# Performance work log

Hardware: AMD Instinct MI355X
Metric: run time of the kernel (lower is better)

## Reference

```python
import jax, jax.numpy as jnp
import numpy as np

EPS = 1e-09


def _glorot(key, shape):
    fan_in, fan_out = shape[-2], shape[-1]
    std = (2.0 / (fan_in + fan_out)) ** 0.5
    return jax.random.normal(key, shape, dtype=jnp.float32) * std


def setup_inputs() -> dict:
    key = jax.random.key(0)
    kx, k1, k2, k3, k4 = jax.random.split(key, 5)
    B, S, D = 2, 1024, 256
    H, K = 8, 32  # key_dim_frac = 1/8
    return {
        "x": jax.random.normal(kx, (B, S, D), dtype=jnp.float32),
        "Wks": _glorot(k1, (H, D, K)),
        "Wqs": _glorot(k2, (H, D, K)),
        "Wvs": _glorot(k3, (H, D, D)),
        "Wo": _glorot(k4, (H, D, D)),
    }


def reference(x, Wks, Wqs, Wvs, Wo):
    # Per-head projections: [H, B, S, K] / [H, B, S, D]
    keys = jnp.einsum('bsd,hdk->hbsk', x, Wks)
    queries = jnp.einsum('bsd,hdk->hbsk', x, Wqs)
    values = jnp.einsum('bsd,hde->hbse', x, Wvs)

    # Feature map: elu + 1 (strictly positive)
    keys = jax.nn.elu(keys) + 1.0
    queries = jax.nn.elu(queries) + 1.0

    # Auxiliary pairwise attention map [H, B, S, S], causal-masked, row-normalized
    att = jnp.einsum('hbsk,hbtk->hbst', queries, keys)
    S = att.shape[-1]
    causal = jnp.tril(jnp.ones((S, S), dtype=att.dtype))
    att = att * causal
    att = att / (jnp.sum(att, axis=-1, keepdims=True) + EPS)

    # Causal linear attention via cumulative sums of outer products
    # [H, B, S, D, K] cumulative state (memory-bound, mirrors tf.cumsum)
    kv = jnp.einsum('hbsk,hbsd->hbsdk', keys, values)
    kv_cum = jnp.cumsum(kv, axis=2)
    numerator = jnp.einsum('hbsdk,hbsk->hbsd', kv_cum, queries)
    denominator = jnp.einsum('hbsk,hbsk->hbs', jnp.cumsum(keys, axis=2), queries)
    node = numerator / (denominator[..., None] + EPS)

    # Output projection, summed over heads: [B, S, D]
    out = jnp.einsum('hbsd,hde->bse', node, Wo)
    return (out, att)
```

## Files before the change

kernel.cpp:

```cpp
#include <hip/hip_runtime.h>
#include <hip/hip_bf16.h>
#include <cstdio>

#define PB 2
#define PS 1024
#define PD 256
#define PK 32
#define PH 8
#define HB (PH*PB)
#define BS (PB*PS)
#define EPS 1e-9f

typedef __attribute__((ext_vector_type(8))) short bf16x8;
typedef __attribute__((ext_vector_type(4))) float f32x4;

__device__ inline unsigned short f2bf(float f) {
    __hip_bfloat16 h = __float2bfloat16(f);
    return *reinterpret_cast<unsigned short*>(&h);
}
__device__ inline float bf2f(unsigned short u) {
    return __bfloat162float(*reinterpret_cast<__hip_bfloat16*>(&u));
}

__global__ __launch_bounds__(256) void k_prep(
    const float* __restrict__ x, const float* __restrict__ Wqs,
    const float* __restrict__ Wks, const float* __restrict__ Wvs,
    const float* __restrict__ Wo,
    unsigned short* __restrict__ xb, unsigned short* __restrict__ WqT,
    unsigned short* __restrict__ WkT, unsigned short* __restrict__ WvT,
    unsigned short* __restrict__ WoT)
{
    __shared__ float smem[8448];
    int bid = blockIdx.x, tid = threadIdx.x;
    if (bid < 512) {
        int i = bid*256 + tid;
        float4 v = ((const float4*)x)[i];
        ushort4 o = {f2bf(v.x), f2bf(v.y), f2bf(v.z), f2bf(v.w)};
        ((ushort4*)xb)[i] = o;
        return;
    }
    if (bid < 528) {
        int r2 = bid - 512;
        int h = r2 >> 1, isK = r2 & 1;
        const float* S = (isK ? Wks : Wqs) + (size_t)h*8192;
        unsigned short* D = (isK ? WkT : WqT) + (size_t)h*8192;
#pragma unroll
        for (int p = 0; p < 32; ++p) {
            int idx = p*256 + tid;
            smem[(idx>>5)*33 + (idx&31)] = S[idx];
        }
        __syncthreads();
#pragma unroll
        for (int p = 0; p < 8; ++p) {
            int o4 = p*256 + tid;
            int kk = o4 >> 6, d = (o4 & 63)*4;
            ushort4 o;
            o.x = f2bf(smem[(d+0)*33 + kk]); o.y = f2bf(smem[(d+1)*33 + kk]);
            o.z = f2bf(smem[(d+2)*33 + kk]); o.w = f2bf(smem[(d+3)*33 + kk]);
            *(ushort4*)(D + (size_t)kk*256 + d) = o;
        }
        return;
    }
    int r3 = bid - 528;
    const float* S; unsigned short* dst; int rs, hs;
    if (r3 < 128) { S = Wvs; dst = WvT; rs = 256;  hs = 65536; }
    else          { r3 -= 128; S = Wo; dst = WoT; rs = 2048; hs = 256; }
    int e0 = (r3 & 3)*64, d0 = ((r3>>2) & 3)*64, h = r3 >> 4;
    float (*T)[69] = (float(*)[69])smem;
    const float* Sh = S + (size_t)h*65536;
    int ty = tid>>4, c4 = tid&15;
#pragma unroll
    for (int p = 0; p < 4; ++p) {
        int r = p*16 + ty;
        float4 v = *(const float4*)(Sh + (size_t)(d0+r)*256 + e0 + c4*4);
        T[r][c4*4+0]=v.x; T[r][c4*4+1]=v.y; T[r][c4*4+2]=v.z; T[r][c4*4+3]=v.w;
    }
    __syncthreads();
    unsigned short* D = dst + (size_t)h*hs;
#pragma unroll
    for (int p = 0; p < 4; ++p) {
        int er = p*16 + ty;
        ushort4 o;
        o.x = f2bf(T[c4*4+0][er]); o.y = f2bf(T[c4*4+1][er]);
        o.z = f2bf(T[c4*4+2][er]); o.w = f2bf(T[c4*4+3][er]);
        *(ushort4*)(D + (size_t)(e0+er)*rs + d0 + c4*4) = o;
    }
}

__global__ __launch_bounds__(256) void k_proj(
    const unsigned short* __restrict__ xb, const unsigned short* __restrict__ WqT,
    const unsigned short* __restrict__ WkT, const unsigned short* __restrict__ WvT,
    unsigned short* __restrict__ Qb, unsigned short* __restrict__ Kb,
    unsigned short* __restrict__ Vt)
{
    int z = blockIdx.z;
    int m0 = blockIdx.y*64, n0 = blockIdx.x*64;
    int tid = threadIdx.x, w = tid>>6, l15 = tid&15, g = (tid>>4)&3;
    f32x4 zf = {0.f,0.f,0.f,0.f};
    f32x4 acc[4] = {zf,zf,zf,zf};
    const unsigned short* arow = xb + (size_t)(m0+16*w+l15)*256 + 8*g;
    const unsigned short* W;
    if (z < 8)       W = WvT + (size_t)z*65536;
    else if (z == 8) W = WqT;
    else             W = WkT;
#pragma unroll
    for (int kk = 0; kk < 8; ++kk) {
        bf16x8 af = *(const bf16x8*)(arow + kk*32);
#pragma unroll
        for (int nt = 0; nt < 4; ++nt) {
            bf16x8 bf = *(const bf16x8*)(W + (size_t)(n0+16*nt+l15)*256 + kk*32 + 8*g);
            acc[nt] = __builtin_amdgcn_mfma_f32_16x16x32_bf16(af, bf, acc[nt], 0, 0, 0);
        }
    }
    if (z < 8) {
        unsigned short* VtT = Vt + ((size_t)z*32 + blockIdx.y)*(256*64);
#pragma unroll
        for (int nt = 0; nt < 4; ++nt) {
            ushort4 o = {f2bf(acc[nt][0]), f2bf(acc[nt][1]), f2bf(acc[nt][2]), f2bf(acc[nt][3])};
            *(ushort4*)(VtT + (size_t)(n0+16*nt+l15)*64 + 16*w + 4*g) = o;
        }
    } else {
        unsigned short* dst = (z == 8) ? Qb : Kb;
        int bs_base = m0 + 16*w + 4*g;
#pragma unroll
        for (int nt = 0; nt < 4; ++nt) {
            int col = n0 + 16*nt + l15;
            int h = col>>5, kk = col&31;
#pragma unroll
            for (int j = 0; j < 4; ++j) {
                int bs = bs_base + j;
                int b = bs>>10, s = bs&1023;
                float zv = acc[nt][j];
                zv = zv > 0.f ? zv + 1.f : expf(zv);
                dst[((size_t)(h*PB+b)*PS + s)*PK + kk] = f2bf(zv);
            }
        }
    }
}

__global__ __launch_bounds__(256) void k_kv_sums(
    const unsigned short* __restrict__ Kb, const unsigned short* __restrict__ Vt,
    float* __restrict__ KVs, float* __restrict__ Ksum)
{
    int c = blockIdx.x, hb = blockIdx.y;
    int tid = threadIdx.x, w = tid>>6, l15 = tid&15, g = (tid>>4)&3;
    __shared__ unsigned short KT[32*72];
    __shared__ float partial[8][32];
#pragma unroll
    for (int i = 0; i < 8; ++i) {
        int flat = tid + i*256;
        KT[(flat&31)*72 + (flat>>5)] = Kb[((size_t)hb*PS + c*64 + (flat>>5))*PK + (flat&31)];
    }
    __syncthreads();
    {
        int kk = tid & 31, part = tid >> 5;
        float s = 0.f;
#pragma unroll
        for (int i = 0; i < 8; ++i) s += bf2f(KT[kk*72 + part*8 + i]);
        partial[part][kk] = s;
    }
    const unsigned short* Vtt = Vt + ((size_t)hb*16 + c)*(256*64);
    f32x4 zf = {0.f,0.f,0.f,0.f};
    f32x4 acc[4][2];
#pragma unroll
    for (int mt = 0; mt < 4; ++mt) { acc[mt][0] = zf; acc[mt][1] = zf; }
#pragma unroll
    for (int ks = 0; ks < 2; ++ks) {
        bf16x8 af[4];
#pragma unroll
        for (int mt = 0; mt < 4; ++mt)
            af[mt] = *(const bf16x8*)(Vtt + (size_t)(64*w + 16*mt + l15)*64 + 32*ks + 8*g);
#pragma unroll
        for (int nt = 0; nt < 2; ++nt) {
            bf16x8 bf = *(const bf16x8*)(KT + (16*nt + l15)*72 + 32*ks + 8*g);
#pragma unroll
            for (int mt = 0; mt < 4; ++mt)
                acc[mt][nt] = __builtin_amdgcn_mfma_f32_16x16x32_bf16(af[mt], bf, acc[mt][nt], 0, 0, 0);
        }
    }
    __syncthreads();
    if (tid < 32) {
        float s = 0.f;
#pragma unroll
        for (int p = 0; p < 8; ++p) s += partial[p][tid];
        Ksum[((size_t)hb*16 + c)*32 + tid] = s;
    }
    float* o = KVs + ((size_t)hb*16 + c)*8192;
#pragma unroll
    for (int mt = 0; mt < 4; ++mt)
#pragma unroll
        for (int nt = 0; nt < 2; ++nt)
#pragma unroll
            for (int j = 0; j < 4; ++j)
                o[(size_t)(64*w + 16*mt + 4*g + j)*32 + 16*nt + l15] = acc[mt][nt][j];
}

__global__ void k_kv_scan(const float* __restrict__ KVs, const float* __restrict__ Ksum,
                          unsigned short* __restrict__ KVpre, float* __restrict__ Kpre) {
    int hb = blockIdx.y;
    if (blockIdx.x == 32) {
        int kk = threadIdx.x;
        if (kk < 32) {
            float acc = 0.f;
#pragma unroll
            for (int c = 0; c < 16; ++c) {
                Kpre[((size_t)hb*16 + c)*32 + kk] = acc;
                acc += Ksum[((size_t)hb*16 + c)*32 + kk];
            }
        }
        return;
    }
    int i = blockIdx.x*256 + threadIdx.x;
    const float* src = KVs + (size_t)hb*16*8192 + i;
    unsigned short* dst = KVpre + (size_t)hb*16*8192 + i;
    float acc = 0.f;
#pragma unroll
    for (int c = 0; c < 16; ++c) { dst[c*8192] = f2bf(acc); acc += src[c*8192]; }
}

__global__ __launch_bounds__(256) void k_den2(
    const unsigned short* __restrict__ Qb, const unsigned short* __restrict__ Kb,
    const float* __restrict__ Kpre, float* __restrict__ den)
{
    int c = blockIdx.x, hb = blockIdx.y;
    int tid = threadIdx.x;
    int r = tid >> 2, quad = tid & 3;
    __shared__ float kc[64][33];
    bf16x8 k8 = *(const bf16x8*)(Kb + ((size_t)hb*PS + c*64 + r)*PK + quad*8);
#pragma unroll
    for (int i = 0; i < 8; ++i) kc[r][quad*8+i] = bf2f((unsigned short)k8[i]);
    __syncthreads();
#pragma unroll
    for (int st = 1; st < 64; st <<= 1) {
        float tmp[8];
#pragma unroll
        for (int i = 0; i < 8; ++i) tmp[i] = (r >= st) ? kc[r-st][quad*8+i] : 0.f;
        __syncthreads();
#pragma unroll
        for (int i = 0; i < 8; ++i) kc[r][quad*8+i] += tmp[i];
        __syncthreads();
    }
    bf16x8 q8 = *(const bf16x8*)(Qb + ((size_t)hb*PS + c*64 + r)*PK + quad*8);
    const float* Kp = Kpre + ((size_t)hb*16 + c)*32 + quad*8;
    float p = 0.f;
#pragma unroll
    for (int i = 0; i < 8; ++i)
        p += bf2f((unsigned short)q8[i]) * (Kp[i] + kc[r][quad*8+i]);
    p += __shfl_xor(p, 1);
    p += __shfl_xor(p, 2);
    if (quad == 0) den[hb*PS + c*64 + r] = p + EPS;
}

__global__ __launch_bounds__(256) void k_att(
    const unsigned short* __restrict__ Qb, const unsigned short* __restrict__ Kb,
    const float* __restrict__ den, float* __restrict__ att)
{
    int st = blockIdx.x, hb = blockIdx.y;
    int s0 = st*64;
    int tid = threadIdx.x, w = tid>>6, l15 = tid&15, g = (tid>>4)&3;

    alignas(16) __shared__ float PT[64][68];
    __shared__ float rden[64];

    float* attb = att + (size_t)hb*PS*PS;
    int c0 = s0 + 64;
    int nzf4 = (PS - c0) >> 2;
    if (nzf4 > 0 && tid < nzf4) {
        float4 z = {0.f,0.f,0.f,0.f};
        float* zb = attb + (size_t)s0*PS + c0 + tid*4;
#pragma unroll 4
        for (int r = 0; r < 64; ++r)
            *(float4*)(zb + (size_t)r*PS) = z;
    }
    if (tid < 64) rden[tid] = 1.0f / den[hb*PS + s0 + tid];

    if (st == 0) return;

    bf16x8 qf = *(const bf16x8*)(Qb + ((size_t)hb*PS + s0 + 16*w + l15)*PK + 8*g);
    f32x4 zf = {0.f,0.f,0.f,0.f};
    __syncthreads();
    float rd[4];
#pragma unroll
    for (int j = 0; j < 4; ++j) rd[j] = rden[16*w + 4*g + j];

    for (int tt = 0; tt < st; ++tt) {
        int t0 = tt*64;
        f32x4 p[4];
#pragma unroll
        for (int nt = 0; nt < 4; ++nt) {
            bf16x8 kf = *(const bf16x8*)(Kb + ((size_t)hb*PS + t0 + 16*nt + l15)*PK + 8*g);
            p[nt] = __builtin_amdgcn_mfma_f32_16x16x32_bf16(qf, kf, zf, 0, 0, 0);
        }
#pragma unroll
        for (int nt = 0; nt < 4; ++nt)
#pragma unroll
            for (int j = 0; j < 4; ++j)
                PT[16*w + 4*g + j][16*nt + l15] = p[nt][j] * rd[j];
        __syncthreads();
#pragma unroll
        for (int pp = 0; pp < 4; ++pp) {
            int f4 = tid + pp*256;
            int r = f4 >> 4, c4 = f4 & 15;
            float4 v = *(const float4*)&PT[r][c4*4];
            *(float4*)(attb + (size_t)(s0+r)*PS + t0 + c4*4) = v;
        }
        __syncthreads();
    }
}

__global__ __launch_bounds__(256) void k_node(
    const unsigned short* __restrict__ Qb, const unsigned short* __restrict__ Kb,
    const float* __restrict__ den, const unsigned short* __restrict__ Vt,
    const unsigned short* __restrict__ KVpre,
    float* __restrict__ att, unsigned short* __restrict__ nodeB)
{
    int c = blockIdx.x, hb = blockIdx.y;
    int s0 = c*64;
    int tid = threadIdx.x, w = tid>>6, l15 = tid&15, g = (tid>>4)&3;
    __shared__ unsigned short PL[64*72];
    __shared__ float rden[64];
    if (tid < 64) rden[tid] = 1.0f / den[hb*PS + s0 + tid];

    f32x4 zf = {0.f,0.f,0.f,0.f};
    bf16x8 qf = *(const bf16x8*)(Qb + ((size_t)hb*PS + s0 + 16*w + l15)*PK + 8*g);

    const unsigned short* KVp = KVpre + ((size_t)hb*16 + c)*8192;
    f32x4 acc[16];
#pragma unroll
    for (int nt = 0; nt < 16; ++nt) {
        bf16x8 bf = *(const bf16x8*)(KVp + (size_t)(16*nt + l15)*32 + 8*g);
        acc[nt] = __builtin_amdgcn_mfma_f32_16x16x32_bf16(qf, bf, zf, 0, 0, 0);
    }
    f32x4 p[4];
#pragma unroll
    for (int nt4 = 0; nt4 < 4; ++nt4) {
        bf16x8 kf = *(const bf16x8*)(Kb + ((size_t)hb*PS + s0 + 16*nt4 + l15)*PK + 8*g);
        p[nt4] = __builtin_amdgcn_mfma_f32_16x16x32_bf16(qf, kf, zf, 0, 0, 0);
    }
    __syncthreads();
    float* attb = att + (size_t)hb*PS*PS;
#pragma unroll
    for (int nt4 = 0; nt4 < 4; ++nt4) {
#pragma unroll
        for (int j = 0; j < 4; ++j) {
            int r = 16*w + 4*g + j;
            int tc = 16*nt4 + l15;
            float v = p[nt4][j] * rden[r];
            if (tc > r) v = 0.f;
            attb[(size_t)(s0 + r)*PS + s0 + tc] = v;
            PL[r*72 + tc] = f2bf(v);
        }
    }
#pragma unroll
    for (int nt = 0; nt < 16; ++nt)
#pragma unroll
        for (int j = 0; j < 4; ++j)
            acc[nt][j] *= rden[16*w + 4*g + j];
    __syncthreads();
    const unsigned short* Vtt = Vt + ((size_t)hb*16 + c)*(256*64);
#pragma unroll
    for (int ks = 0; ks < 2; ++ks) {
        bf16x8 af = *(const bf16x8*)(PL + (size_t)(16*w + l15)*72 + 32*ks + 8*g);
#pragma unroll
        for (int nt = 0; nt < 16; ++nt) {
            bf16x8 vf = *(const bf16x8*)(Vtt + (size_t)(16*nt + l15)*64 + 32*ks + 8*g);
            acc[nt] = __builtin_amdgcn_mfma_f32_16x16x32_bf16(af, vf, acc[nt], 0, 0, 0);
        }
    }
    int h = hb >> 1, b = hb & 1;
    unsigned short* np = nodeB + ((size_t)(b*PS + s0))*2048 + h*256;
#pragma unroll
    for (int nt = 0; nt < 16; ++nt)
#pragma unroll
        for (int j = 0; j < 4; ++j)
            np[(size_t)(16*w + 4*g + j)*2048 + 16*nt + l15] = f2bf(acc[nt][j]);
}

__global__ __launch_bounds__(256) void k_out2(
    const unsigned short* __restrict__ nodeB, const unsigned short* __restrict__ WoT,
    float* __restrict__ out)
{
    int e0 = blockIdx.x*64, m0 = blockIdx.y*16;
    int tid = threadIdx.x, w = tid>>6, l15 = tid&15, g = (tid>>4)&3;
    f32x4 zf = {0.f,0.f,0.f,0.f};
    f32x4 acc = zf;
    const unsigned short* arow = nodeB + (size_t)(m0 + l15)*2048 + 8*g;
    const unsigned short* brow = WoT + (size_t)(e0 + 16*w + l15)*2048 + 8*g;
#pragma unroll 8
    for (int kk = 0; kk < 64; ++kk) {
        bf16x8 af = *(const bf16x8*)(arow + kk*32);
        bf16x8 bf = *(const bf16x8*)(brow + kk*32);
        acc = __builtin_amdgcn_mfma_f32_16x16x32_bf16(af, bf, acc, 0, 0, 0);
    }
#pragma unroll
    for (int j = 0; j < 4; ++j)
        out[(size_t)(m0 + 4*g + j)*PD + e0 + 16*w + l15] = acc[j];
}

extern "C" void kernel_launch(void* const* d_in, const int* in_sizes, int n_in,
                              void* d_out, int out_size, void* d_ws, size_t ws_size,
                              hipStream_t stream) {
    const float* x   = (const float*)d_in[0];
    const float* Wks = (const float*)d_in[1];
    const float* Wqs = (const float*)d_in[2];
    const float* Wvs = (const float*)d_in[3];
    const float* Wo  = (const float*)d_in[4];

    float* out = (float*)d_out;
    float* att = (float*)d_out + (size_t)PB*PS*PD;

    float* ws = (float*)d_ws;
    float*          den   = ws + 0;
    unsigned short* Qb    = (unsigned short*)(ws + 16384);
    unsigned short* Kb    = (unsigned short*)(ws + 278528);
    unsigned short* Vt    = (unsigned short*)(ws + 540672);
    unsigned short* xb    = (unsigned short*)(ws + 2637824);
    unsigned short* WqT   = (unsigned short*)(ws + 2899968);
    unsigned short* WkT   = (unsigned short*)(ws + 2932736);
    unsigned short* WvT   = (unsigned short*)(ws + 2965504);
    unsigned short* WoT   = (unsigned short*)(ws + 3227648);
    unsigned short* nodeB = (unsigned short*)(ws + 3489792);
    float*          KVs   = ws + 5586944;
    unsigned short* KVpre = (unsigned short*)(ws + 7684096);
    float*          KsumG = ws + 8732672;
    float*          KpreG = ws + 8740864;
    const size_t needed = (size_t)8749056 * 4;
    if (ws_size < needed) {
        fprintf(stderr, "kernel_launch: ws_size %zu < needed %zu\n", ws_size, needed);
        return;
    }

    k_prep<<<784, 256, 0, stream>>>(x, Wqs, Wks, Wvs, Wo, xb, WqT, WkT, WvT, WoT);
    k_proj<<<dim3(4, 32, 10), 256, 0, stream>>>(xb, WqT, WkT, WvT, Qb, Kb, Vt);
    k_kv_sums<<<dim3(16, HB), 256, 0, stream>>>(Kb, Vt, KVs, KsumG);
    k_kv_scan<<<dim3(33, HB), 256, 0, stream>>>(KVs, KsumG, KVpre, KpreG);
    k_den2<<<dim3(16, HB), 256, 0, stream>>>(Qb, Kb, KpreG, den);
    k_att<<<dim3(16, HB), 256, 0, stream>>>(Qb, Kb, den, att);
    k_node<<<dim3(16, HB), 256, 0, stream>>>(Qb, Kb, den, Vt, KVpre, att, nodeB);
    k_out2<<<dim3(4, 128), 256, 0, stream>>>(nodeB, WoT, out);
}
```

Baseline: 102.9 us.

## Fuse post-projection kernels into one cooperative megakernel with grid syncs

Replaces six separate launches (kv sums, kv scan, denominator, attention map, node, output projection) with a single cooperative kernel of 256 blocks of 512 threads, using grid.sync between the phases. Denominators stay in shared memory instead of going through global memory, the K prefix is computed by each block directly from the chunk sums, and the diagonal attention tile is written once alongside the bf16 copy. The intent is to remove launch overhead and inter-kernel gaps. In exchange it adds grid-wide barrier costs and a fixed, possibly poorly balanced work split, since causal attention blocks carry uneven amounts of work.

```diff
diff --git a/kernel.cpp b/kernel.cpp
--- a/kernel.cpp
+++ b/kernel.cpp
@@ -1,6 +1,9 @@
 #include <hip/hip_runtime.h>
 #include <hip/hip_bf16.h>
+#include <hip/hip_cooperative_groups.h>
 #include <cstdio>
+
+namespace cg = cooperative_groups;
 
 #define PB 2
 #define PS 1024
@@ -138,263 +141,265 @@
     }
 }
 
-__global__ __launch_bounds__(256) void k_kv_sums(
-    const unsigned short* __restrict__ Kb, const unsigned short* __restrict__ Vt,
-    float* __restrict__ KVs, float* __restrict__ Ksum)
+__global__ __launch_bounds__(512) void k_mega(
+    const unsigned short* __restrict__ Qb, const unsigned short* __restrict__ Kb,
+    const unsigned short* __restrict__ Vt,
+    float* __restrict__ KVs, float* __restrict__ KsumG,
+    unsigned short* __restrict__ KVpre,
+    float* __restrict__ att, unsigned short* __restrict__ nodeB,
+    const unsigned short* __restrict__ WoT, float* __restrict__ out)
 {
+    cg::grid_group grid = cg::this_grid();
     int c = blockIdx.x, hb = blockIdx.y;
-    int tid = threadIdx.x, w = tid>>6, l15 = tid&15, g = (tid>>4)&3;
-    __shared__ unsigned short KT[32*72];
-    __shared__ float partial[8][32];
-#pragma unroll
-    for (int i = 0; i < 8; ++i) {
-        int flat = tid + i*256;
+    int tid = threadIdx.x;
+    int w = tid >> 6, l15 = tid & 15, g = (tid >> 4) & 3;
+    f32x4 zf = {0.f, 0.f, 0.f, 0.f};
+
+    __shared__ __align__(16) unsigned char smem[26880];
+    unsigned short* PL   = (unsigned short*)smem;
+    float* rden          = (float*)(smem + 9216);
+    unsigned short* KT   = (unsigned short*)(smem + 9472);
+    float* partial       = (float*)(smem + 9472 + 4608);
+    float (*kc)[33]      = (float(*)[33])(smem + 9472);
+    float (*PT)[68]      = (float(*)[68])(smem + 9472);
+
+    const unsigned short* Vtt = Vt + ((size_t)hb*16 + c)*(256*64);
+
+#pragma unroll
+    for (int i = 0; i < 4; ++i) {
+        int flat = tid + i*512;
         KT[(flat&31)*72 + (flat>>5)] = Kb[((size_t)hb*PS + c*64 + (flat>>5))*PK + (flat&31)];
     }
     __syncthreads();
-    {
+    if (tid < 256) {
         int kk = tid & 31, part = tid >> 5;
         float s = 0.f;
 #pragma unroll
         for (int i = 0; i < 8; ++i) s += bf2f(KT[kk*72 + part*8 + i]);
-        partial[part][kk] = s;
-    }
-    const unsigned short* Vtt = Vt + ((size_t)hb*16 + c)*(256*64);
-    f32x4 zf = {0.f,0.f,0.f,0.f};
-    f32x4 acc[4][2];
-#pragma unroll
-    for (int mt = 0; mt < 4; ++mt) { acc[mt][0] = zf; acc[mt][1] = zf; }
-#pragma unroll
-    for (int ks = 0; ks < 2; ++ks) {
-        bf16x8 af[4];
-#pragma unroll
-        for (int mt = 0; mt < 4; ++mt)
-            af[mt] = *(const bf16x8*)(Vtt + (size_t)(64*w + 16*mt + l15)*64 + 32*ks + 8*g);
-#pragma unroll
-        for (int nt = 0; nt < 2; ++nt) {
-            bf16x8 bf = *(const bf16x8*)(KT + (16*nt + l15)*72 + 32*ks + 8*g);
-#pragma unroll
-            for (int mt = 0; mt < 4; ++mt)
-                acc[mt][nt] = __builtin_amdgcn_mfma_f32_16x16x32_bf16(af[mt], bf, acc[mt][nt], 0, 0, 0);
-        }
-    }
-    __syncthreads();
-    if (tid < 32) {
-        float s = 0.f;
-#pragma unroll
-        for (int p = 0; p < 8; ++p) s += partial[p][tid];
-        Ksum[((size_t)hb*16 + c)*32 + tid] = s;
-    }
-    float* o = KVs + ((size_t)hb*16 + c)*8192;
-#pragma unroll
-    for (int mt = 0; mt < 4; ++mt)
-#pragma unroll
-        for (int nt = 0; nt < 2; ++nt)
+        partial[part*32 + kk] = s;
+    }
+    {
+        f32x4 acc1[2][2];
+        acc1[0][0]=zf; acc1[0][1]=zf; acc1[1][0]=zf; acc1[1][1]=zf;
+#pragma unroll
+        for (int ks = 0; ks < 2; ++ks) {
+            bf16x8 af[2];
+#pragma unroll
+            for (int mt = 0; mt < 2; ++mt)
+                af[mt] = *(const bf16x8*)(Vtt + (size_t)(32*w + 16*mt + l15)*64 + 32*ks + 8*g);
+#pragma unroll
+            for (int nt = 0; nt < 2; ++nt) {
+                bf16x8 bf = *(const bf16x8*)(KT + (16*nt + l15)*72 + 32*ks + 8*g);
+#pragma unroll
+                for (int mt = 0; mt < 2; ++mt)
+                    acc1[mt][nt] = __builtin_amdgcn_mfma_f32_16x16x32_bf16(af[mt], bf, acc1[mt][nt], 0, 0, 0);
+            }
+        }
+        __syncthreads();
+        if (tid < 32) {
+            float s = 0.f;
+#pragma unroll
+            for (int p = 0; p < 8; ++p) s += partial[p*32 + tid];
+            KsumG[((size_t)hb*16 + c)*32 + tid] = s;
+        }
+        float* o = KVs + ((size_t)hb*16 + c)*8192;
+#pragma unroll
+        for (int mt = 0; mt < 2; ++mt)
+#pragma unroll
+            for (int nt = 0; nt < 2; ++nt)
+#pragma unroll
+                for (int j = 0; j < 4; ++j)
+                    o[(size_t)(32*w + 16*mt + 4*g + j)*32 + 16*nt + l15] = acc1[mt][nt][j];
+    }
+    grid.sync();
+
+    {
+        int i = c*512 + tid;
+        const float* src = KVs + (size_t)hb*16*8192 + i;
+        unsigned short* dst = KVpre + (size_t)hb*16*8192 + i;
+        float acc = 0.f;
+#pragma unroll
+        for (int cc = 0; cc < 16; ++cc) { dst[cc*8192] = f2bf(acc); acc += src[cc*8192]; }
+    }
+    grid.sync();
+
+    {
+        bool act = tid < 256;
+        int r = tid >> 2, quad = tid & 3;
+        if (act) {
+            bf16x8 k8 = *(const bf16x8*)(Kb + ((size_t)hb*PS + c*64 + r)*PK + quad*8);
+#pragma unroll
+            for (int i = 0; i < 8; ++i) kc[r][quad*8+i] = bf2f((unsigned short)k8[i]);
+        }
+        __syncthreads();
+#pragma unroll
+        for (int st = 1; st < 64; st <<= 1) {
+            float tmp[8];
+            if (act) {
+#pragma unroll
+                for (int i = 0; i < 8; ++i) tmp[i] = (r >= st) ? kc[r-st][quad*8+i] : 0.f;
+            }
+            __syncthreads();
+            if (act) {
+#pragma unroll
+                for (int i = 0; i < 8; ++i) kc[r][quad*8+i] += tmp[i];
+            }
+            __syncthreads();
+        }
+        if (act) {
+            float kp[8];
+#pragma unroll
+            for (int i = 0; i < 8; ++i) kp[i] = 0.f;
+            for (int cc = 0; cc < c; ++cc) {
+                const float* Ks = KsumG + ((size_t)hb*16 + cc)*32 + quad*8;
+#pragma unroll
+                for (int i = 0; i < 8; ++i) kp[i] += Ks[i];
+            }
+            bf16x8 q8 = *(const bf16x8*)(Qb + ((size_t)hb*PS + c*64 + r)*PK + quad*8);
+            float p = 0.f;
+#pragma unroll
+            for (int i = 0; i < 8; ++i)
+                p += bf2f((unsigned short)q8[i]) * (kp[i] + kc[r][quad*8+i]);
+            p += __shfl_xor(p, 1);
+            p += __shfl_xor(p, 2);
+            if (quad == 0) rden[r] = 1.0f / (p + EPS);
+        }
+        __syncthreads();
+    }
+
+    int s0 = c*64;
+    float* attb = att + (size_t)hb*PS*PS;
+    {
+        int c0 = s0 + 64;
+        int nzf4 = (PS - c0) >> 2;
+        int col = tid & 255, half = tid >> 8;
+        if (col < nzf4) {
+            float4 z = {0.f,0.f,0.f,0.f};
+            float* zb = attb + (size_t)(s0 + 32*half)*PS + c0 + col*4;
+#pragma unroll 4
+            for (int r = 0; r < 32; ++r)
+                *(float4*)(zb + (size_t)r*PS) = z;
+        }
+        int ws = w & 3, eh = w >> 2;
+        bf16x8 qf = *(const bf16x8*)(Qb + ((size_t)hb*PS + s0 + 16*ws + l15)*PK + 8*g);
+        float rd[4];
+#pragma unroll
+        for (int j = 0; j < 4; ++j) rd[j] = rden[16*ws + 4*g + j];
+        for (int tt = 0; tt < c; ++tt) {
+            int t0 = tt*64;
+            f32x4 p[2];
+#pragma unroll
+            for (int i = 0; i < 2; ++i) {
+                int nt = eh*2 + i;
+                bf16x8 kf = *(const bf16x8*)(Kb + ((size_t)hb*PS + t0 + 16*nt + l15)*PK + 8*g);
+                p[i] = __builtin_amdgcn_mfma_f32_16x16x32_bf16(qf, kf, zf, 0, 0, 0);
+            }
+#pragma unroll
+            for (int i = 0; i < 2; ++i) {
+                int nt = eh*2 + i;
+#pragma unroll
+                for (int j = 0; j < 4; ++j)
+                    PT[16*ws + 4*g + j][16*nt + l15] = p[i][j] * rd[j];
+            }
+            __syncthreads();
+#pragma unroll
+            for (int pp = 0; pp < 2; ++pp) {
+                int f4 = tid + pp*512;
+                int r = f4 >> 4, c4 = f4 & 15;
+                float4 v = *(const float4*)&PT[r][c4*4];
+                *(float4*)(attb + (size_t)(s0+r)*PS + t0 + c4*4) = v;
+            }
+            __syncthreads();
+        }
+        {
+            f32x4 p[2];
+#pragma unroll
+            for (int i = 0; i < 2; ++i) {
+                int nt = eh*2 + i;
+                bf16x8 kf = *(const bf16x8*)(Kb + ((size_t)hb*PS + s0 + 16*nt + l15)*PK + 8*g);
+                p[i] = __builtin_amdgcn_mfma_f32_16x16x32_bf16(qf, kf, zf, 0, 0, 0);
+            }
+#pragma unroll
+            for (int i = 0; i < 2; ++i) {
+                int nt = eh*2 + i;
+                int tc = 16*nt + l15;
+#pragma unroll
+                for (int j = 0; j < 4; ++j) {
+                    int r = 16*ws + 4*g + j;
+                    float v = p[i][j] * rd[j];
+                    if (tc > r) v = 0.f;
+                    PT[r][tc] = v;
+                    PL[r*72 + tc] = f2bf(v);
+                }
+            }
+            __syncthreads();
+#pragma unroll
+            for (int pp = 0; pp < 2; ++pp) {
+                int f4 = tid + pp*512;
+                int r = f4 >> 4, c4 = f4 & 15;
+                float4 v = *(const float4*)&PT[r][c4*4];
+                *(float4*)(attb + (size_t)(s0+r)*PS + s0 + c4*4) = v;
+            }
+            __syncthreads();
+        }
+    }
+
+    {
+        int ws = w & 3, eh = w >> 2;
+        bf16x8 qf = *(const bf16x8*)(Qb + ((size_t)hb*PS + s0 + 16*ws + l15)*PK + 8*g);
+        const unsigned short* KVp = KVpre + ((size_t)hb*16 + c)*8192;
+        f32x4 acc[8];
+#pragma unroll
+        for (int nt = 0; nt < 8; ++nt) {
+            int tile = eh*8 + nt;
+            bf16x8 bf = *(const bf16x8*)(KVp + (size_t)(16*tile + l15)*32 + 8*g);
+            acc[nt] = __builtin_amdgcn_mfma_f32_16x16x32_bf16(qf, bf, zf, 0, 0, 0);
+        }
+        float rd[4];
+#pragma unroll
+        for (int j = 0; j < 4; ++j) rd[j] = rden[16*ws + 4*g + j];
+#pragma unroll
+        for (int nt = 0; nt < 8; ++nt)
+#pragma unroll
+            for (int j = 0; j < 4; ++j) acc[nt][j] *= rd[j];
+#pragma unroll
+        for (int ks = 0; ks < 2; ++ks) {
+            bf16x8 af = *(const bf16x8*)(PL + (size_t)(16*ws + l15)*72 + 32*ks + 8*g);
+#pragma unroll
+            for (int nt = 0; nt < 8; ++nt) {
+                int tile = eh*8 + nt;
+                bf16x8 vf = *(const bf16x8*)(Vtt + (size_t)(16*tile + l15)*64 + 32*ks + 8*g);
+                acc[nt] = __builtin_amdgcn_mfma_f32_16x16x32_bf16(af, vf, acc[nt], 0, 0, 0);
+            }
+        }
+        int h = hb >> 1, b = hb & 1;
+        unsigned short* np = nodeB + ((size_t)(b*PS + s0))*2048 + h*256;
+#pragma unroll
+        for (int nt = 0; nt < 8; ++nt)
 #pragma unroll
             for (int j = 0; j < 4; ++j)
-                o[(size_t)(64*w + 16*mt + 4*g + j)*32 + 16*nt + l15] = acc[mt][nt][j];
-}
-
-__global__ void k_kv_scan(const float* __restrict__ KVs, const float* __restrict__ Ksum,
-                          unsigned short* __restrict__ KVpre, float* __restrict__ Kpre) {
-    int hb = blockIdx.y;
-    if (blockIdx.x == 32) {
-        int kk = threadIdx.x;
-        if (kk < 32) {
-            float acc = 0.f;
-#pragma unroll
-            for (int c = 0; c < 16; ++c) {
-                Kpre[((size_t)hb*16 + c)*32 + kk] = acc;
-                acc += Ksum[((size_t)hb*16 + c)*32 + kk];
-            }
-        }
-        return;
-    }
-    int i = blockIdx.x*256 + threadIdx.x;
-    const float* src = KVs + (size_t)hb*16*8192 + i;
-    unsigned short* dst = KVpre + (size_t)hb*16*8192 + i;
-    float acc = 0.f;
-#pragma unroll
-    for (int c = 0; c < 16; ++c) { dst[c*8192] = f2bf(acc); acc += src[c*8192]; }
-}
-
-__global__ __launch_bounds__(256) void k_den2(
-    const unsigned short* __restrict__ Qb, const unsigned short* __restrict__ Kb,
-    const float* __restrict__ Kpre, float* __restrict__ den)
-{
-    int c = blockIdx.x, hb = blockIdx.y;
-    int tid = threadIdx.x;
-    int r = tid >> 2, quad = tid & 3;
-    __shared__ float kc[64][33];
-    bf16x8 k8 = *(const bf16x8*)(Kb + ((size_t)hb*PS + c*64 + r)*PK + quad*8);
-#pragma unroll
-    for (int i = 0; i < 8; ++i) kc[r][quad*8+i] = bf2f((unsigned short)k8[i]);
-    __syncthreads();
-#pragma unroll
-    for (int st = 1; st < 64; st <<= 1) {
-        float tmp[8];
-#pragma unroll
-        for (int i = 0; i < 8; ++i) tmp[i] = (r >= st) ? kc[r-st][quad*8+i] : 0.f;
-        __syncthreads();
-#pragma unroll
-        for (int i = 0; i < 8; ++i) kc[r][quad*8+i] += tmp[i];
-        __syncthreads();
-    }
-    bf16x8 q8 = *(const bf16x8*)(Qb + ((size_t)hb*PS + c*64 + r)*PK + quad*8);
-    const float* Kp = Kpre + ((size_t)hb*16 + c)*32 + quad*8;
-    float p = 0.f;
-#pragma unroll
-    for (int i = 0; i < 8; ++i)
-        p += bf2f((unsigned short)q8[i]) * (Kp[i] + kc[r][quad*8+i]);
-    p += __shfl_xor(p, 1);
-    p += __shfl_xor(p, 2);
-    if (quad == 0) den[hb*PS + c*64 + r] = p + EPS;
-}
-
-__global__ __launch_bounds__(256) void k_att(
-    const unsigned short* __restrict__ Qb, const unsigned short* __restrict__ Kb,
-    const float* __restrict__ den, float* __restrict__ att)
-{
-    int st = blockIdx.x, hb = blockIdx.y;
-    int s0 = st*64;
-    int tid = threadIdx.x, w = tid>>6, l15 = tid&15, g = (tid>>4)&3;
-
-    alignas(16) __shared__ float PT[64][68];
-    __shared__ float rden[64];
-
-    float* attb = att + (size_t)hb*PS*PS;
-    int c0 = s0 + 64;
-    int nzf4 = (PS - c0) >> 2;
-    if (nzf4 > 0 && tid < nzf4) {
-        float4 z = {0.f,0.f,0.f,0.f};
-        float* zb = attb + (size_t)s0*PS + c0 + tid*4;
-#pragma unroll 4
-        for (int r = 0; r < 64; ++r)
-            *(float4*)(zb + (size_t)r*PS) = z;
-    }
-    if (tid < 64) rden[tid] = 1.0f / den[hb*PS + s0 + tid];
-
-    if (st == 0) return;
-
-    bf16x8 qf = *(const bf16x8*)(Qb + ((size_t)hb*PS + s0 + 16*w + l15)*PK + 8*g);
-    f32x4 zf = {0.f,0.f,0.f,0.f};
-    __syncthreads();
-    float rd[4];
-#pragma unroll
-    for (int j = 0; j < 4; ++j) rd[j] = rden[16*w + 4*g + j];
-
-    for (int tt = 0; tt < st; ++tt) {
-        int t0 = tt*64;
-        f32x4 p[4];
-#pragma unroll
-        for (int nt = 0; nt < 4; ++nt) {
-            bf16x8 kf = *(const bf16x8*)(Kb + ((size_t)hb*PS + t0 + 16*nt + l15)*PK + 8*g);
-            p[nt] = __builtin_amdgcn_mfma_f32_16x16x32_bf16(qf, kf, zf, 0, 0, 0);
-        }
-#pragma unroll
-        for (int nt = 0; nt < 4; ++nt)
-#pragma unroll
-            for (int j = 0; j < 4; ++j)
-                PT[16*w + 4*g + j][16*nt + l15] = p[nt][j] * rd[j];
-        __syncthreads();
-#pragma unroll
-        for (int pp = 0; pp < 4; ++pp) {
-            int f4 = tid + pp*256;
-            int r = f4 >> 4, c4 = f4 & 15;
-            float4 v = *(const float4*)&PT[r][c4*4];
-            *(float4*)(attb + (size_t)(s0+r)*PS + t0 + c4*4) = v;
-        }
-        __syncthreads();
-    }
-}
-
-__global__ __launch_bounds__(256) void k_node(
-    const unsigned short* __restrict__ Qb, const unsigned short* __restrict__ Kb,
-    const float* __restrict__ den, const unsigned short* __restrict__ Vt,
-    const unsigned short* __restrict__ KVpre,
-    float* __restrict__ att, unsigned short* __restrict__ nodeB)
-{
-    int c = blockIdx.x, hb = blockIdx.y;
-    int s0 = c*64;
-    int tid = threadIdx.x, w = tid>>6, l15 = tid&15, g = (tid>>4)&3;
-    __shared__ unsigned short PL[64*72];
-    __shared__ float rden[64];
-    if (tid < 64) rden[tid] = 1.0f / den[hb*PS + s0 + tid];
-
-    f32x4 zf = {0.f,0.f,0.f,0.f};
-    bf16x8 qf = *(const bf16x8*)(Qb + ((size_t)hb*PS + s0 + 16*w + l15)*PK + 8*g);
-
-    const unsigned short* KVp = KVpre + ((size_t)hb*16 + c)*8192;
-    f32x4 acc[16];
-#pragma unroll
-    for (int nt = 0; nt < 16; ++nt) {
-        bf16x8 bf = *(const bf16x8*)(KVp + (size_t)(16*nt + l15)*32 + 8*g);
-        acc[nt] = __builtin_amdgcn_mfma_f32_16x16x32_bf16(qf, bf, zf, 0, 0, 0);
-    }
-    f32x4 p[4];
-#pragma unroll
-    for (int nt4 = 0; nt4 < 4; ++nt4) {
-        bf16x8 kf = *(const bf16x8*)(Kb + ((size_t)hb*PS + s0 + 16*nt4 + l15)*PK + 8*g);
-        p[nt4] = __builtin_amdgcn_mfma_f32_16x16x32_bf16(qf, kf, zf, 0, 0, 0);
-    }
-    __syncthreads();
-    float* attb = att + (size_t)hb*PS*PS;
-#pragma unroll
-    for (int nt4 = 0; nt4 < 4; ++nt4) {
-#pragma unroll
-        for (int j = 0; j < 4; ++j) {
-            int r = 16*w + 4*g + j;
-            int tc = 16*nt4 + l15;
-            float v = p[nt4][j] * rden[r];
-            if (tc > r) v = 0.f;
-            attb[(size_t)(s0 + r)*PS + s0 + tc] = v;
-            PL[r*72 + tc] = f2bf(v);
-        }
-    }
-#pragma unroll
-    for (int nt = 0; nt < 16; ++nt)
+                np[(size_t)(16*ws + 4*g + j)*2048 + 16*(eh*8 + nt) + l15] = f2bf(acc[nt][j]);
+    }
+    grid.sync();
+
+    {
+        int t = (blockIdx.y*16 + blockIdx.x)*2 + (tid >> 8);
+        int e0 = (t & 3)*64, m0 = (t >> 2)*16;
+        int tid2 = tid & 255;
+        int w2 = tid2 >> 6, l15b = tid2 & 15, g2 = (tid2 >> 4) & 3;
+        f32x4 acc = zf;
+        const unsigned short* arow = nodeB + (size_t)(m0 + l15b)*2048 + 8*g2;
+        const unsigned short* brow = WoT + (size_t)(e0 + 16*w2 + l15b)*2048 + 8*g2;
+#pragma unroll 8
+        for (int kk = 0; kk < 64; ++kk) {
+            bf16x8 af = *(const bf16x8*)(arow + kk*32);
+            bf16x8 bf = *(const bf16x8*)(brow + kk*32);
+            acc = __builtin_amdgcn_mfma_f32_16x16x32_bf16(af, bf, acc, 0, 0, 0);
+        }
 #pragma unroll
         for (int j = 0; j < 4; ++j)
-            acc[nt][j] *= rden[16*w + 4*g + j];
-    __syncthreads();
-    const unsigned short* Vtt = Vt + ((size_t)hb*16 + c)*(256*64);
-#pragma unroll
-    for (int ks = 0; ks < 2; ++ks) {
-        bf16x8 af = *(const bf16x8*)(PL + (size_t)(16*w + l15)*72 + 32*ks + 8*g);
-#pragma unroll
-        for (int nt = 0; nt < 16; ++nt) {
-            bf16x8 vf = *(const bf16x8*)(Vtt + (size_t)(16*nt + l15)*64 + 32*ks + 8*g);
-            acc[nt] = __builtin_amdgcn_mfma_f32_16x16x32_bf16(af, vf, acc[nt], 0, 0, 0);
-        }
-    }
-    int h = hb >> 1, b = hb & 1;
-    unsigned short* np = nodeB + ((size_t)(b*PS + s0))*2048 + h*256;
-#pragma unroll
-    for (int nt = 0; nt < 16; ++nt)
-#pragma unroll
-        for (int j = 0; j < 4; ++j)
-            np[(size_t)(16*w + 4*g + j)*2048 + 16*nt + l15] = f2bf(acc[nt][j]);
-}
-
-__global__ __launch_bounds__(256) void k_out2(
-    const unsigned short* __restrict__ nodeB, const unsigned short* __restrict__ WoT,
-    float* __restrict__ out)
-{
-    int e0 = blockIdx.x*64, m0 = blockIdx.y*16;
-    int tid = threadIdx.x, w = tid>>6, l15 = tid&15, g = (tid>>4)&3;
-    f32x4 zf = {0.f,0.f,0.f,0.f};
-    f32x4 acc = zf;
-    const unsigned short* arow = nodeB + (size_t)(m0 + l15)*2048 + 8*g;
-    const unsigned short* brow = WoT + (size_t)(e0 + 16*w + l15)*2048 + 8*g;
-#pragma unroll 8
-    for (int kk = 0; kk < 64; ++kk) {
-        bf16x8 af = *(const bf16x8*)(arow + kk*32);
-        bf16x8 bf = *(const bf16x8*)(brow + kk*32);
-        acc = __builtin_amdgcn_mfma_f32_16x16x32_bf16(af, bf, acc, 0, 0, 0);
-    }
-#pragma unroll
-    for (int j = 0; j < 4; ++j)
-        out[(size_t)(m0 + 4*g + j)*PD + e0 + 16*w + l15] = acc[j];
+            out[(size_t)(m0 + 4*g2 + j)*PD + e0 + 16*w2 + l15b] = acc[j];
+    }
 }
 
 extern "C" void kernel_launch(void* const* d_in, const int* in_sizes, int n_in,
@@ -410,21 +415,19 @@
     float* att = (float*)d_out + (size_t)PB*PS*PD;
 
     float* ws = (float*)d_ws;
-    float*          den   = ws + 0;
-    unsigned short* Qb    = (unsigned short*)(ws + 16384);
-    unsigned short* Kb    = (unsigned short*)(ws + 278528);
-    unsigned short* Vt    = (unsigned short*)(ws + 540672);
-    unsigned short* xb    = (unsigned short*)(ws + 2637824);
-    unsigned short* WqT   = (unsigned short*)(ws + 2899968);
-    unsigned short* WkT   = (unsigned short*)(ws + 2932736);
-    unsigned short* WvT   = (unsigned short*)(ws + 2965504);
-    unsigned short* WoT   = (unsigned short*)(ws + 3227648);
-    unsigned short* nodeB = (unsigned short*)(ws + 3489792);
-    float*          KVs   = ws + 5586944;
-    unsigned short* KVpre = (unsigned short*)(ws + 7684096);
-    float*          KsumG = ws + 8732672;
-    float*          KpreG = ws + 8740864;
-    const size_t needed = (size_t)8749056 * 4;
+    unsigned short* Qb    = (unsigned short*)(ws + 0);
+    unsigned short* Kb    = (unsigned short*)(ws + 262144);
+    unsigned short* Vt    = (unsigned short*)(ws + 524288);
+    unsigned short* xb    = (unsigned short*)(ws + 2621440);
+    unsigned short* WqT   = (unsigned short*)(ws + 2883584);
+    unsigned short* WkT   = (unsigned short*)(ws + 2916352);
+    unsigned short* WvT   = (unsigned short*)(ws + 2949120);
+    unsigned short* WoT   = (unsigned short*)(ws + 3211264);
+    unsigned short* nodeB = (unsigned short*)(ws + 3473408);
+    float*          KVs   = ws + 5570560;
+    unsigned short* KVpre = (unsigned short*)(ws + 7667712);
+    float*          KsumG = ws + 8716288;
+    const size_t needed = (size_t)8724480 * 4;
     if (ws_size < needed) {
         fprintf(stderr, "kernel_launch: ws_size %zu < needed %zu\n", ws_size, needed);
         return;
@@ -432,10 +435,12 @@
 
     k_prep<<<784, 256, 0, stream>>>(x, Wqs, Wks, Wvs, Wo, xb, WqT, WkT, WvT, WoT);
     k_proj<<<dim3(4, 32, 10), 256, 0, stream>>>(xb, WqT, WkT, WvT, Qb, Kb, Vt);
-    k_kv_sums<<<dim3(16, HB), 256, 0, stream>>>(Kb, Vt, KVs, KsumG);
-    k_kv_scan<<<dim3(33, HB), 256, 0, stream>>>(KVs, KsumG, KVpre, KpreG);
-    k_den2<<<dim3(16, HB), 256, 0, stream>>>(Qb, Kb, KpreG, den);
-    k_att<<<dim3(16, HB), 256, 0, stream>>>(Qb, Kb, den, att);
-    k_node<<<dim3(16, HB), 256, 0, stream>>>(Qb, Kb, den, Vt, KVpre, att, nodeB);
-    k_out2<<<dim3(4, 128), 256, 0, stream>>>(nodeB, WoT, out);
-}
+
+    void* kargs[] = {
+        (void*)&Qb, (void*)&Kb, (void*)&Vt,
+        (void*)&KVs, (void*)&KsumG, (void*)&KVpre,
+        (void*)&att, (void*)&nodeB, (void*)&WoT, (void*)&out
+    };
+    hipLaunchCooperativeKernel((void*)k_mega, dim3(16, 16), dim3(512, 1, 1),
+                               kargs, 0, stream);
+}
```

Result: slower. 203.8 us (+98.1%).

## Merge KV scan with denominator and attention with node kernels into tile grid

Applied to the files above, without the earlier changes.

Fuses the KV prefix scan and the denominator computation into one kernel, with each denominator block recomputing its own K-sum prefix instead of reading a separately scanned array. Also merges the attention-map and node kernels into one launch over a 3D grid where each block handles a single 64x64 attention tile (zero, off-diagonal, or diagonal plus node). This cuts two kernel launches and spreads the serial per-row-tile loop of the old attention kernel across many blocks for better parallelism. The cost is more small blocks, each reloading Q and den, and a short serial Ksum loop per block.

```diff
diff --git a/kernel.cpp b/kernel.cpp
--- a/kernel.cpp
+++ b/kernel.cpp
@@ -195,37 +195,26 @@
                 o[(size_t)(64*w + 16*mt + 4*g + j)*32 + 16*nt + l15] = acc[mt][nt][j];
 }
 
-__global__ void k_kv_scan(const float* __restrict__ KVs, const float* __restrict__ Ksum,
-                          unsigned short* __restrict__ KVpre, float* __restrict__ Kpre) {
+__global__ __launch_bounds__(256) void k_mid(
+    const float* __restrict__ KVs, const float* __restrict__ Ksum,
+    const unsigned short* __restrict__ Qb, const unsigned short* __restrict__ Kb,
+    unsigned short* __restrict__ KVpre, float* __restrict__ den)
+{
     int hb = blockIdx.y;
-    if (blockIdx.x == 32) {
-        int kk = threadIdx.x;
-        if (kk < 32) {
-            float acc = 0.f;
-#pragma unroll
-            for (int c = 0; c < 16; ++c) {
-                Kpre[((size_t)hb*16 + c)*32 + kk] = acc;
-                acc += Ksum[((size_t)hb*16 + c)*32 + kk];
-            }
-        }
+    int xb_ = blockIdx.x;
+    __shared__ float kc[64][33];
+    if (xb_ < 32) {
+        int i = xb_*256 + threadIdx.x;
+        const float* src = KVs + (size_t)hb*16*8192 + i;
+        unsigned short* dst = KVpre + (size_t)hb*16*8192 + i;
+        float acc = 0.f;
+#pragma unroll
+        for (int cc = 0; cc < 16; ++cc) { dst[cc*8192] = f2bf(acc); acc += src[cc*8192]; }
         return;
     }
-    int i = blockIdx.x*256 + threadIdx.x;
-    const float* src = KVs + (size_t)hb*16*8192 + i;
-    unsigned short* dst = KVpre + (size_t)hb*16*8192 + i;
-    float acc = 0.f;
-#pragma unroll
-    for (int c = 0; c < 16; ++c) { dst[c*8192] = f2bf(acc); acc += src[c*8192]; }
-}
-
-__global__ __launch_bounds__(256) void k_den2(
-    const unsigned short* __restrict__ Qb, const unsigned short* __restrict__ Kb,
-    const float* __restrict__ Kpre, float* __restrict__ den)
-{
-    int c = blockIdx.x, hb = blockIdx.y;
+    int c = xb_ - 32;
     int tid = threadIdx.x;
     int r = tid >> 2, quad = tid & 3;
-    __shared__ float kc[64][33];
     bf16x8 k8 = *(const bf16x8*)(Kb + ((size_t)hb*PS + c*64 + r)*PK + quad*8);
 #pragma unroll
     for (int i = 0; i < 8; ++i) kc[r][quad*8+i] = bf2f((unsigned short)k8[i]);
@@ -240,50 +229,56 @@
         for (int i = 0; i < 8; ++i) kc[r][quad*8+i] += tmp[i];
         __syncthreads();
     }
+    float kp[8];
+#pragma unroll
+    for (int i = 0; i < 8; ++i) kp[i] = 0.f;
+    for (int cc = 0; cc < c; ++cc) {
+        const float* Ks = Ksum + ((size_t)hb*16 + cc)*32 + quad*8;
+#pragma unroll
+        for (int i = 0; i < 8; ++i) kp[i] += Ks[i];
+    }
     bf16x8 q8 = *(const bf16x8*)(Qb + ((size_t)hb*PS + c*64 + r)*PK + quad*8);
-    const float* Kp = Kpre + ((size_t)hb*16 + c)*32 + quad*8;
     float p = 0.f;
 #pragma unroll
     for (int i = 0; i < 8; ++i)
-        p += bf2f((unsigned short)q8[i]) * (Kp[i] + kc[r][quad*8+i]);
+        p += bf2f((unsigned short)q8[i]) * (kp[i] + kc[r][quad*8+i]);
     p += __shfl_xor(p, 1);
     p += __shfl_xor(p, 2);
     if (quad == 0) den[hb*PS + c*64 + r] = p + EPS;
 }
 
-__global__ __launch_bounds__(256) void k_att(
+__global__ __launch_bounds__(256) void k_att_node(
     const unsigned short* __restrict__ Qb, const unsigned short* __restrict__ Kb,
-    const float* __restrict__ den, float* __restrict__ att)
-{
-    int st = blockIdx.x, hb = blockIdx.y;
+    const float* __restrict__ den, const unsigned short* __restrict__ Vt,
+    const unsigned short* __restrict__ KVpre,
+    float* __restrict__ att, unsigned short* __restrict__ nodeB)
+{
+    int tt = blockIdx.x, st = blockIdx.y, hb = blockIdx.z;
     int s0 = st*64;
     int tid = threadIdx.x, w = tid>>6, l15 = tid&15, g = (tid>>4)&3;
-
-    alignas(16) __shared__ float PT[64][68];
-    __shared__ float rden[64];
-
     float* attb = att + (size_t)hb*PS*PS;
-    int c0 = s0 + 64;
-    int nzf4 = (PS - c0) >> 2;
-    if (nzf4 > 0 && tid < nzf4) {
-        float4 z = {0.f,0.f,0.f,0.f};
-        float* zb = attb + (size_t)s0*PS + c0 + tid*4;
-#pragma unroll 4
-        for (int r = 0; r < 64; ++r)
-            *(float4*)(zb + (size_t)r*PS) = z;
-    }
-    if (tid < 64) rden[tid] = 1.0f / den[hb*PS + s0 + tid];
-
-    if (st == 0) return;
-
-    bf16x8 qf = *(const bf16x8*)(Qb + ((size_t)hb*PS + s0 + 16*w + l15)*PK + 8*g);
     f32x4 zf = {0.f,0.f,0.f,0.f};
-    __syncthreads();
-    float rd[4];
-#pragma unroll
-    for (int j = 0; j < 4; ++j) rd[j] = rden[16*w + 4*g + j];
-
-    for (int tt = 0; tt < st; ++tt) {
+
+    __shared__ __align__(16) unsigned char smem[17664];
+    float (*PT)[68] = (float(*)[68])smem;
+    unsigned short* PL = (unsigned short*)smem;
+    float* rden = (float*)(smem + 17408);
+
+    if (tt < 16) {
+        if (tt == st) return;
+        if (tt > st) {
+            float4 z = {0.f,0.f,0.f,0.f};
+            float* base = attb + (size_t)s0*PS + tt*64;
+#pragma unroll
+            for (int pp = 0; pp < 4; ++pp) {
+                int f4 = tid + pp*256;
+                int r = f4 >> 4, c4 = f4 & 15;
+                *(float4*)(base + (size_t)r*PS + c4*4) = z;
+            }
+            return;
+        }
+        if (tid < 64) rden[tid] = 1.0f / den[hb*PS + s0 + tid];
+        bf16x8 qf = *(const bf16x8*)(Qb + ((size_t)hb*PS + s0 + 16*w + l15)*PK + 8*g);
         int t0 = tt*64;
         f32x4 p[4];
 #pragma unroll
@@ -291,6 +286,10 @@
             bf16x8 kf = *(const bf16x8*)(Kb + ((size_t)hb*PS + t0 + 16*nt + l15)*PK + 8*g);
             p[nt] = __builtin_amdgcn_mfma_f32_16x16x32_bf16(qf, kf, zf, 0, 0, 0);
         }
+        __syncthreads();
+        float rd[4];
+#pragma unroll
+        for (int j = 0; j < 4; ++j) rd[j] = rden[16*w + 4*g + j];
 #pragma unroll
         for (int nt = 0; nt < 4; ++nt)
 #pragma unroll
@@ -304,26 +303,12 @@
             float4 v = *(const float4*)&PT[r][c4*4];
             *(float4*)(attb + (size_t)(s0+r)*PS + t0 + c4*4) = v;
         }
-        __syncthreads();
-    }
-}
-
-__global__ __launch_bounds__(256) void k_node(
-    const unsigned short* __restrict__ Qb, const unsigned short* __restrict__ Kb,
-    const float* __restrict__ den, const unsigned short* __restrict__ Vt,
-    const unsigned short* __restrict__ KVpre,
-    float* __restrict__ att, unsigned short* __restrict__ nodeB)
-{
-    int c = blockIdx.x, hb = blockIdx.y;
-    int s0 = c*64;
-    int tid = threadIdx.x, w = tid>>6, l15 = tid&15, g = (tid>>4)&3;
-    __shared__ unsigned short PL[64*72];
-    __shared__ float rden[64];
+        return;
+    }
+
+    int c = st;
     if (tid < 64) rden[tid] = 1.0f / den[hb*PS + s0 + tid];
-
-    f32x4 zf = {0.f,0.f,0.f,0.f};
     bf16x8 qf = *(const bf16x8*)(Qb + ((size_t)hb*PS + s0 + 16*w + l15)*PK + 8*g);
-
     const unsigned short* KVp = KVpre + ((size_t)hb*16 + c)*8192;
     f32x4 acc[16];
 #pragma unroll
@@ -338,7 +323,6 @@
         p[nt4] = __builtin_amdgcn_mfma_f32_16x16x32_bf16(qf, kf, zf, 0, 0, 0);
     }
     __syncthreads();
-    float* attb = att + (size_t)hb*PS*PS;
 #pragma unroll
     for (int nt4 = 0; nt4 < 4; ++nt4) {
 #pragma unroll
@@ -423,8 +407,7 @@
     float*          KVs   = ws + 5586944;
     unsigned short* KVpre = (unsigned short*)(ws + 7684096);
     float*          KsumG = ws + 8732672;
-    float*          KpreG = ws + 8740864;
-    const size_t needed = (size_t)8749056 * 4;
+    const size_t needed = (size_t)8740864 * 4;
     if (ws_size < needed) {
         fprintf(stderr, "kernel_launch: ws_size %zu < needed %zu\n", ws_size, needed);
         return;
@@ -433,9 +416,7 @@
     k_prep<<<784, 256, 0, stream>>>(x, Wqs, Wks, Wvs, Wo, xb, WqT, WkT, WvT, WoT);
     k_proj<<<dim3(4, 32, 10), 256, 0, stream>>>(xb, WqT, WkT, WvT, Qb, Kb, Vt);
     k_kv_sums<<<dim3(16, HB), 256, 0, stream>>>(Kb, Vt, KVs, KsumG);
-    k_kv_scan<<<dim3(33, HB), 256, 0, stream>>>(KVs, KsumG, KVpre, KpreG);
-    k_den2<<<dim3(16, HB), 256, 0, stream>>>(Qb, Kb, KpreG, den);
-    k_att<<<dim3(16, HB), 256, 0, stream>>>(Qb, Kb, den, att);
-    k_node<<<dim3(16, HB), 256, 0, stream>>>(Qb, Kb, den, Vt, KVpre, att, nodeB);
+    k_mid<<<dim3(48, HB), 256, 0, stream>>>(KVs, KsumG, Qb, Kb, KVpre, den);
+    k_att_node<<<dim3(17, 16, HB), 256, 0, stream>>>(Qb, Kb, den, Vt, KVpre, att, nodeB);
     k_out2<<<dim3(4, 128), 256, 0, stream>>>(nodeB, WoT, out);
 }
```

After: 102.3 us. Within noise of the previous version (-0.5%).
